# Performance work log

Hardware: AMD Instinct MI355X
Metric: run time of the kernel (lower is better)

The kernel has to match this reference:

```python
import jax, jax.numpy as jnp
import numpy as np

HIDDEN = 96
INF = 1e30


def setup_inputs() -> dict:
    key = jax.random.key(0)
    ks = jax.random.split(key, 9)
    B, JX, JM, D_IN, D_MEM = 8, 2048, 2048, 150, 150
    GATED = D_IN + D_MEM  # 300
    inputs = jax.random.normal(ks[0], (B, JX, D_IN), dtype=jnp.float32)
    memory = jax.random.normal(ks[1], (B, JM, D_MEM), dtype=jnp.float32)
    mask = jax.random.randint(ks[2], (B, JM), 0, 2, dtype=jnp.int32)
    s_in = 1.0 / np.sqrt(D_IN)
    s_g = 1.0 / np.sqrt(GATED)
    Wi = jax.random.uniform(ks[3], (D_IN, HIDDEN), jnp.float32, -s_in, s_in)
    bi = jax.random.uniform(ks[4], (HIDDEN,), jnp.float32, -s_in, s_in)
    Wm = jax.random.uniform(ks[5], (D_MEM, HIDDEN), jnp.float32, -s_in, s_in)
    bm = jax.random.uniform(ks[6], (HIDDEN,), jnp.float32, -s_in, s_in)
    Wg = jax.random.uniform(ks[7], (GATED, GATED), jnp.float32, -s_g, s_g)
    bg = jax.random.uniform(ks[8], (GATED,), jnp.float32, -s_g, s_g)
    return {"inputs": inputs, "memory": memory, "mask": mask,
            "Wi": Wi, "bi": bi, "Wm": Wm, "bm": bm, "Wg": Wg, "bg": bg}


def reference(inputs, memory, mask, Wi, bi, Wm, bm, Wg, bg):
    # ReLU projections (inference mode: dropout is identity)
    inputs_ = jax.nn.relu(jnp.einsum('bxd,dh->bxh', inputs, Wi) + bi)  # [B,JX,H]
    memory_ = jax.nn.relu(jnp.einsum('byd,dh->byh', memory, Wm) + bm)  # [B,JM,H]
    # Scaled dot-product scores [B,JX,JM]
    scores = jnp.einsum('bxh,byh->bxy', inputs_, memory_) / jnp.sqrt(
        jnp.asarray(HIDDEN, inputs.dtype))
    # Additive mask: -INF where mask==0 (broadcast over JX)
    maskf = mask.astype(inputs.dtype)[:, None, :]  # [B,1,JM]
    scores = scores - INF * (1.0 - maskf)
    logits = jax.nn.softmax(scores, axis=-1)
    outputs = jnp.einsum('bxy,byd->bxd', logits, memory)  # [B,JX,D_MEM]
    res = jnp.concatenate([inputs, outputs], axis=2)  # [B,JX,GATED]
    gate = jax.nn.sigmoid(jnp.einsum('bxg,gk->bxk', res, Wg) + bg)
    return gate * res
```

## Files before the change

### kernel.cpp

```cpp
#include <hip/hip_runtime.h>

#define BB 8
#define JX 2048
#define JMDIM 2048
#define DID 150
#define HID 96
#define GATED 300
#define NSPLIT 2
#define NROWS (BB * JX)

typedef unsigned short u16;
typedef __attribute__((ext_vector_type(8))) short bh8;
typedef __attribute__((ext_vector_type(4))) float f32x4;

#define SCALE2    (0.14724444f)

__device__ inline float b2f(u16 u) {
    union { unsigned int i; float f; } c; c.i = ((unsigned int)u) << 16; return c.f;
}
__device__ inline u16 f2b(float f) {
    unsigned int u = __float_as_uint(f);
    unsigned int r = (u + 0x7fffu + ((u >> 16) & 1u)) >> 16;
    return (u16)r;
}

__global__ __launch_bounds__(256) void proj2_kernel(
    const float* __restrict__ inputs, const float* __restrict__ memory,
    const int* __restrict__ mask,
    const float* __restrict__ Wi, const float* __restrict__ bi,
    const float* __restrict__ Wm, const float* __restrict__ bm,
    const float* __restrict__ Wg,
    u16* __restrict__ Qp, u16* __restrict__ Xi,
    u16* __restrict__ Kp, u16* __restrict__ Vt,
    u16* __restrict__ Wgt, int* __restrict__ mcount) {
    __shared__ __align__(16) u16 Xl[64 * 168];
    __shared__ __align__(16) u16 Wl[96 * 168];
    __shared__ int Il[64];
    __shared__ int wsum[4];
    const int tid = threadIdx.x;

    if (blockIdx.y == 2) {
        int t = blockIdx.x * 256 + tid;
        for (int e = t; e < 304 * 328; e += 256 * 256) {
            int k = e / 328, d = e - k * 328;
            Wgt[e] = (k < GATED && d < GATED) ? f2b(Wg[d * GATED + k]) : (u16)0;
        }
        return;
    }

    if (blockIdx.y == 0) {
        size_t row0 = (size_t)blockIdx.x * 64;
        const float4* Xv = (const float4*)(inputs + row0 * DID);
        for (int i = tid; i < 2400; i += 256) {
            float4 v = Xv[i];
            int base = i * 4;
#pragma unroll
            for (int k = 0; k < 4; ++k) {
                int id = base + k;
                int r = id / DID, d = id - r * DID;
                Xl[r * 168 + d] = f2b(((const float*)&v)[k]);
            }
        }
        for (int e = tid; e < 64 * 18; e += 256) {
            int r = e / 18, d = 150 + (e - r * 18);
            Xl[r * 168 + d] = 0;
        }
        for (int e = tid; e < 96 * 168; e += 256) {
            int h = e / 168, d = e - h * 168;
            Wl[e] = (d < DID) ? f2b(Wi[d * HID + h]) : (u16)0;
        }
        __syncthreads();

        for (int e = tid; e < 64 * 20; e += 256) {
            int r = e / 20, c = e - r * 20;
            *(bh8*)(Xi + (row0 + r) * 160 + c * 8) = *(const bh8*)(Xl + r * 168 + c * 8);
        }

        int wave = tid >> 6, lane = tid & 63, quad = lane >> 4, l15 = lane & 15;
        bh8 af[5];
#pragma unroll
        for (int kc = 0; kc < 5; ++kc)
            af[kc] = *(const bh8*)(Xl + (wave * 16 + l15) * 168 + kc * 32 + quad * 8);
#pragma unroll
        for (int nt = 0; nt < 6; ++nt) {
            f32x4 acc = {0.f, 0.f, 0.f, 0.f};
#pragma unroll
            for (int kc = 0; kc < 5; ++kc) {
                bh8 bf = *(const bh8*)(Wl + (nt * 16 + l15) * 168 + kc * 32 + quad * 8);
                acc = __builtin_amdgcn_mfma_f32_16x16x32_bf16(af[kc], bf, acc, 0, 0, 0);
            }
            int h = nt * 16 + l15;
            float bv = bi[h];
#pragma unroll
            for (int j = 0; j < 4; ++j) {
                float y = acc[j] + bv;
                y = y > 0.f ? y : 0.f;
                Qp[(row0 + wave * 16 + quad * 4 + j) * HID + h] = f2b(y);
            }
        }
        return;
    }

    const int b = blockIdx.x >> 5, s = blockIdx.x & 31;
    const int jc0 = s * 64;

    const int* m = mask + (size_t)b * JMDIM;
    int v[8], cnt = 0;
#pragma unroll
    for (int k = 0; k < 8; ++k) { v[k] = m[tid * 8 + k]; cnt += v[k]; }
    {
        int lane = tid & 63, wave = tid >> 6;
        int sc = cnt;
        for (int off = 1; off < 64; off <<= 1) {
            int t = __shfl_up(sc, off, 64);
            if (lane >= off) sc += t;
        }
        if (lane == 63) wsum[wave] = sc;
        if (tid < 64) Il[tid] = -1;
        __syncthreads();
        int wbase = 0;
        for (int w = 0; w < wave; ++w) wbase += wsum[w];
        int base = wbase + sc - cnt;
        int mc_ = wsum[0] + wsum[1] + wsum[2] + wsum[3];
        if (s == 0 && tid == 0) mcount[b] = mc_;
        int p = base;
#pragma unroll
        for (int k = 0; k < 8; ++k) {
            if (v[k]) {
                unsigned off = (unsigned)(p - jc0);
                if (off < 64u) Il[off] = tid * 8 + k;
                ++p;
            }
        }
        for (int e = tid; e < 96 * 168; e += 256) {
            int h = e / 168, d = e - h * 168;
            Wl[e] = (d < DID) ? f2b(Wm[d * HID + h]) : (u16)0;
        }
        __syncthreads();
        const int ntiles = (mc_ + 63) >> 6;
        if (s >= ntiles) return;
    }
    const int mc = wsum[0] + wsum[1] + wsum[2] + wsum[3];

    const float* Mb = memory + (size_t)b * JMDIM * DID;
    for (int e = tid; e < 64 * 75; e += 256) {
        int r = e / 75, c = e - r * 75;
        int row = Il[r];
        float2 val = make_float2(0.f, 0.f);
        if (row >= 0) val = *(const float2*)(Mb + (size_t)row * DID + c * 2);
        Xl[r * 168 + c * 2]     = f2b(val.x);
        Xl[r * 168 + c * 2 + 1] = f2b(val.y);
    }
    for (int e = tid; e < 64 * 18; e += 256) {
        int r = e / 18, d = 150 + (e - r * 18);
        Xl[r * 168 + d] = 0;
    }
    __syncthreads();

    for (int e = tid; e < 160 * 64; e += 256) {
        int d = e >> 6, c = e & 63;
        int jc = jc0 + c;
        u16 vv;
        if (d < DID)       vv = Xl[c * 168 + d];
        else if (d == DID) vv = (jc < mc) ? (u16)0x3F80 : (u16)0;
        else               vv = 0;
        Vt[((size_t)b * 160 + d) * JMDIM + jc] = vv;
    }

    int wave = tid >> 6, lane = tid & 63, quad = lane >> 4, l15 = lane & 15;
    bh8 af[5];
#pragma unroll
    for (int kc = 0; kc < 5; ++kc)
        af[kc] = *(const bh8*)(Xl + (wave * 16 + l15) * 168 + kc * 32 + quad * 8);
#pragma unroll
    for (int nt = 0; nt < 6; ++nt) {
        f32x4 acc = {0.f, 0.f, 0.f, 0.f};
#pragma unroll
        for (int kc = 0; kc < 5; ++kc) {
            bh8 bf = *(const bh8*)(Wl + (nt * 16 + l15) * 168 + kc * 32 + quad * 8);
            acc = __builtin_amdgcn_mfma_f32_16x16x32_bf16(af[kc], bf, acc, 0, 0, 0);
        }
        int h = nt * 16 + l15;
        float bv = bm[h];
#pragma unroll
        for (int j = 0; j < 4; ++j) {
            float y = acc[j] + bv;
            y = y > 0.f ? y : 0.f;
            Kp[((size_t)b * JMDIM + jc0 + wave * 16 + quad * 4 + j) * HID + h] = f2b(y);
        }
    }
}

template <int SPLIT>
__global__ __launch_bounds__(256, 2) void attn_kernel(
    const u16* __restrict__ Qp, const u16* __restrict__ Kp,
    const u16* __restrict__ Vt, const int* __restrict__ mcount,
    u16* __restrict__ Opart, float* __restrict__ lpart) {
    __shared__ __align__(16) u16 Kl[64 * 104];
    __shared__ __align__(16) u16 Vl[160 * 72];
    __shared__ __align__(16) u16 Pl[128 * 72];
    const int b = blockIdx.y;
    const int x0 = blockIdx.x * 128;
    const int tid = threadIdx.x;
    const int wave = tid >> 6, lane = tid & 63;
    const int quad = lane >> 4, l15 = lane & 15;

    const int mc = mcount[b];
    const int ntiles = (mc + 63) >> 6;
    const int zi = blockIdx.z;
    const int myT = (ntiles > zi) ? ((ntiles - 1 - zi) / SPLIT + 1) : 0;

    bh8 qf[2][3];
#pragma unroll
    for (int mt = 0; mt < 2; ++mt) {
        const u16* qb = Qp + ((size_t)b * JX + x0 + wave * 32 + mt * 16 + l15) * HID + quad * 8;
        qf[mt][0] = *(const bh8*)(qb);
        qf[mt][1] = *(const bh8*)(qb + 32);
        qf[mt][2] = *(const bh8*)(qb + 64);
    }

    f32x4 o[2][10];
    const f32x4 zero4 = {0.f, 0.f, 0.f, 0.f};
#pragma unroll
    for (int mt = 0; mt < 2; ++mt)
#pragma unroll
        for (int i = 0; i < 10; ++i) o[mt][i] = zero4;

    const int jm0_0 = zi * 64;

    const u16* kptr[3]; u16* kdst[3];
#pragma unroll
    for (int t = 0; t < 3; ++t) {
        int i = tid + t * 256, r = i / 12, c = i - r * 12;
        kptr[t] = Kp + ((size_t)b * JMDIM + jm0_0 + r) * HID + c * 8;
        kdst[t] = Kl + r * 104 + c * 8;
    }
    const u16* vptr[5]; u16* vdst[5];
#pragma unroll
    for (int t = 0; t < 5; ++t) {
        int i = tid + t * 256, d = i >> 3, c = i & 7;
        vptr[t] = Vt + ((size_t)b * 160 + d) * JMDIM + jm0_0 + c * 8;
        vdst[t] = Vl + d * 72 + c * 8;
    }

    bh8 kreg[3], vreg[5];
    if (myT > 0) {
#pragma unroll
        for (int t = 0; t < 3; ++t) { kreg[t] = *(const bh8*)kptr[t]; kptr[t] += SPLIT * 64 * HID; }
#pragma unroll
        for (int t = 0; t < 5; ++t) { vreg[t] = *(const bh8*)vptr[t]; vptr[t] += SPLIT * 64; }
    }

    for (int it = 0; it < myT; ++it) {
        __syncthreads();
#pragma unroll
        for (int t = 0; t < 3; ++t) *(bh8*)kdst[t] = kreg[t];
#pragma unroll
        for (int t = 0; t < 5; ++t) *(bh8*)vdst[t] = vreg[t];
        if (it + 1 < myT) {
#pragma unroll
            for (int t = 0; t < 3; ++t) { kreg[t] = *(const bh8*)kptr[t]; kptr[t] += SPLIT * 64 * HID; }
#pragma unroll
            for (int t = 0; t < 5; ++t) { vreg[t] = *(const bh8*)vptr[t]; vptr[t] += SPLIT * 64; }
        }
        __syncthreads();

        f32x4 s[2][4];
#pragma unroll
        for (int mt = 0; mt < 2; ++mt)
#pragma unroll
            for (int nt = 0; nt < 4; ++nt) s[mt][nt] = zero4;
#pragma unroll
        for (int nt = 0; nt < 4; ++nt) {
#pragma unroll
            for (int kc = 0; kc < 3; ++kc) {
                bh8 bf = *(const bh8*)(Kl + (nt * 16 + l15) * 104 + kc * 32 + quad * 8);
                s[0][nt] = __builtin_amdgcn_mfma_f32_16x16x32_bf16(qf[0][kc], bf, s[0][nt], 0, 0, 0);
                s[1][nt] = __builtin_amdgcn_mfma_f32_16x16x32_bf16(qf[1][kc], bf, s[1][nt], 0, 0, 0);
            }
        }
#pragma unroll
        for (int nt = 0; nt < 4; ++nt) {
#pragma unroll
            for (int mt = 0; mt < 2; ++mt)
#pragma unroll
                for (int j = 0; j < 4; ++j) {
                    float p = __builtin_amdgcn_exp2f(s[mt][nt][j] * SCALE2);
                    Pl[(wave * 32 + mt * 16 + quad * 4 + j) * 72 + nt * 16 + l15] = f2b(p);
                }
        }
        __threadfence_block();

        bh8 pf[2][2];
#pragma unroll
        for (int mt = 0; mt < 2; ++mt) {
            pf[mt][0] = *(const bh8*)(Pl + (wave * 32 + mt * 16 + l15) * 72 + quad * 8);
            pf[mt][1] = *(const bh8*)(Pl + (wave * 32 + mt * 16 + l15) * 72 + 32 + quad * 8);
        }
#pragma unroll
        for (int nt = 0; nt < 10; ++nt) {
#pragma unroll
            for (int kc = 0; kc < 2; ++kc) {
                bh8 bf = *(const bh8*)(Vl + (nt * 16 + l15) * 72 + kc * 32 + quad * 8);
                o[0][nt] = __builtin_amdgcn_mfma_f32_16x16x32_bf16(pf[0][kc], bf, o[0][nt], 0, 0, 0);
                o[1][nt] = __builtin_amdgcn_mfma_f32_16x16x32_bf16(pf[1][kc], bf, o[1][nt], 0, 0, 0);
            }
        }
    }

    const size_t z = blockIdx.z;
    const int srcLane = (lane & 48) | 6;
#pragma unroll
    for (int mt = 0; mt < 2; ++mt) {
        float lv[4], inv[4];
#pragma unroll
        for (int j = 0; j < 4; ++j) {
            lv[j] = __shfl(o[mt][9][j], srcLane, 64);
            inv[j] = (lv[j] > 0.f) ? 1.f / lv[j] : 0.f;
        }
        size_t grow = (size_t)b * JX + x0 + wave * 32 + mt * 16;
#pragma unroll
        for (int nt = 0; nt < 10; ++nt) {
            int d = nt * 16 + l15;
            if (d < 152) {
#pragma unroll
                for (int j = 0; j < 4; ++j)
                    Opart[(z * NROWS + grow + quad * 4 + j) * 152 + d] = f2b(o[mt][nt][j] * inv[j]);
            }
        }
        if (l15 == 0) {
#pragma unroll
            for (int j = 0; j < 4; ++j)
                lpart[z * NROWS + grow + quad * 4 + j] = lv[j];
        }
    }
}

template <int SPLIT>
__global__ __launch_bounds__(256) void gate_kernel(
    const u16* __restrict__ Xi, const u16* __restrict__ Opart,
    const float* __restrict__ lpart,
    const u16* __restrict__ Wgt, const float* __restrict__ bg,
    float* __restrict__ out) {
    __shared__ __align__(16) u16 Rl[32 * 328];
    __shared__ float Cw[SPLIT * 32];
    int tid = threadIdx.x;
    size_t row0 = (size_t)blockIdx.x * 32;

    if (tid < 32) {
        float l[SPLIT], L = 0.f;
#pragma unroll
        for (int s = 0; s < SPLIT; ++s) {
            l[s] = lpart[(size_t)s * NROWS + row0 + tid];
            L += l[s];
        }
        float invL = (L > 0.f) ? 1.f / L : 0.f;
#pragma unroll
        for (int s = 0; s < SPLIT; ++s) Cw[s * 32 + tid] = l[s] * invL;
    }
    for (int e = tid; e < 32 * 20; e += 256) {
        int r = e / 20, c = e - r * 20;
        *(bh8*)(Rl + r * 328 + c * 8) = *(const bh8*)(Xi + (row0 + r) * 160 + c * 8);
    }
    __syncthreads();
    for (int e = tid; e < 32 * 19; e += 256) {
        int r = e / 19, q = e - r * 19;
        float acc[8];
#pragma unroll
        for (int k = 0; k < 8; ++k) acc[k] = 0.f;
#pragma unroll
        for (int s = 0; s < SPLIT; ++s) {
            bh8 v = *(const bh8*)(Opart + ((size_t)s * NROWS + row0 + r) * 152 + q * 8);
            float w = Cw[s * 32 + r];
#pragma unroll
            for (int k = 0; k < 8; ++k) acc[k] += b2f(((const u16*)&v)[k]) * w;
        }
        u16* dst = Rl + r * 328 + 150 + q * 8;
#pragma unroll
        for (int k = 0; k < 8; ++k) dst[k] = f2b(acc[k]);
    }
    for (int e = tid; e < 32 * 26; e += 256) {
        int r = e / 26, c = 302 + (e - r * 26);
        Rl[r * 328 + c] = 0;
    }
    __syncthreads();

    int wave = tid >> 6, lane = tid & 63, quad = lane >> 4, l15 = lane & 15;
    bh8 af[2][10];
#pragma unroll
    for (int mt = 0; mt < 2; ++mt)
#pragma unroll
        for (int kc = 0; kc < 10; ++kc)
            af[mt][kc] = *(const bh8*)(Rl + (mt * 16 + l15) * 328 + kc * 32 + quad * 8);
    for (int nt = wave; nt < 19; nt += 4) {
        int h = nt * 16 + l15;
        f32x4 acc0 = {0.f, 0.f, 0.f, 0.f};
        f32x4 acc1 = {0.f, 0.f, 0.f, 0.f};
#pragma unroll
        for (int kc = 0; kc < 10; ++kc) {
            bh8 bf = *(const bh8*)(Wgt + (size_t)h * 328 + kc * 32 + quad * 8);
            acc0 = __builtin_amdgcn_mfma_f32_16x16x32_bf16(af[0][kc], bf, acc0, 0, 0, 0);
            acc1 = __builtin_amdgcn_mfma_f32_16x16x32_bf16(af[1][kc], bf, acc1, 0, 0, 0);
        }
        if (h < GATED) {
            float bv = bg[h];
#pragma unroll
            for (int j = 0; j < 4; ++j) {
                int r0 = quad * 4 + j;
                float x0 = acc0[j] + bv;
                float g0 = 1.f / (1.f + __expf(-x0));
                out[(row0 + r0) * GATED + h] = g0 * b2f(Rl[r0 * 328 + h]);
                int r1 = r0 + 16;
                float x1 = acc1[j] + bv;
                float g1 = 1.f / (1.f + __expf(-x1));
                out[(row0 + r1) * GATED + h] = g1 * b2f(Rl[r1 * 328 + h]);
            }
        }
    }
}

extern "C" void kernel_launch(void* const* d_in, const int* in_sizes, int n_in,
                              void* d_out, int out_size, void* d_ws, size_t ws_size,
                              hipStream_t stream) {
    const float* inputs = (const float*)d_in[0];
    const float* memory = (const float*)d_in[1];
    const int*   mask   = (const int*)d_in[2];
    const float* Wi = (const float*)d_in[3];
    const float* bi = (const float*)d_in[4];
    const float* Wm = (const float*)d_in[5];
    const float* bm = (const float*)d_in[6];
    const float* Wg = (const float*)d_in[7];
    const float* bg = (const float*)d_in[8];
    float* out = (float*)d_out;

    u16* Qp  = (u16*)d_ws;
    u16* Kp  = Qp + (size_t)NROWS * HID;
    u16* Vt  = Kp + (size_t)NROWS * HID;
    u16* Xi  = Vt + (size_t)BB * 160 * JMDIM;
    u16* Wgt = Xi + (size_t)NROWS * 160;
    u16* Opart = Wgt + 304 * 328;
    size_t u16_elems = (size_t)(Opart - Qp) + (size_t)NSPLIT * NROWS * 152;
    size_t base_bytes = ((u16_elems * sizeof(u16)) + 15) & ~(size_t)15;
    float* lpart = (float*)((char*)d_ws + base_bytes);
    int* mcountp = (int*)(lpart + (size_t)NSPLIT * NROWS);
    size_t needed = base_bytes + (size_t)NSPLIT * NROWS * sizeof(float)
                  + BB * sizeof(int);
    if (ws_size < needed) return;

    proj2_kernel<<<dim3(256, 3), 256, 0, stream>>>(
        inputs, memory, mask, Wi, bi, Wm, bm, Wg,
        Qp, Xi, Kp, Vt, Wgt, mcountp);
    attn_kernel<NSPLIT><<<dim3(JX / 128, BB, NSPLIT), 256, 0, stream>>>(
        Qp, Kp, Vt, mcountp, Opart, lpart);
    gate_kernel<NSPLIT><<<dim3(NROWS / 32), 256, 0, stream>>>(
        Xi, Opart, lpart, Wgt, bg, out);
}
```

Before: 150.9 us.

## Halve attention query tile to 64 rows and coalesce weight loads in projection

The attention kernel now processes 64 query rows per block (one 16-row MFMA tile per wave) instead of 128, doubling the grid and halving per-wave registers and P shared memory. This aims to raise occupancy and spread work over more CUs, at the cost of loading each K/V tile twice as often per query row. The projection kernel now reads Wi/Wm row-major (coalesced) and scatters the transpose into LDS with a separate padding loop. exp2 also switches from the builtin to exp2f.

```diff
diff --git a/kernel.cpp b/kernel.cpp
--- a/kernel.cpp
+++ b/kernel.cpp
@@ -65,9 +65,13 @@
             int r = e / 18, d = 150 + (e - r * 18);
             Xl[r * 168 + d] = 0;
         }
-        for (int e = tid; e < 96 * 168; e += 256) {
-            int h = e / 168, d = e - h * 168;
-            Wl[e] = (d < DID) ? f2b(Wi[d * HID + h]) : (u16)0;
+        for (int e = tid; e < DID * HID; e += 256) {
+            int d = e / HID, h = e - d * HID;
+            Wl[h * 168 + d] = f2b(Wi[e]);
+        }
+        for (int e = tid; e < HID * 18; e += 256) {
+            int h = e / 18, d = 150 + (e - h * 18);
+            Wl[h * 168 + d] = 0;
         }
         __syncthreads();
 
@@ -108,6 +112,7 @@
     int v[8], cnt = 0;
 #pragma unroll
     for (int k = 0; k < 8; ++k) { v[k] = m[tid * 8 + k]; cnt += v[k]; }
+    int mc;
     {
         int lane = tid & 63, wave = tid >> 6;
         int sc = cnt;
@@ -121,8 +126,8 @@
         int wbase = 0;
         for (int w = 0; w < wave; ++w) wbase += wsum[w];
         int base = wbase + sc - cnt;
-        int mc_ = wsum[0] + wsum[1] + wsum[2] + wsum[3];
-        if (s == 0 && tid == 0) mcount[b] = mc_;
+        mc = wsum[0] + wsum[1] + wsum[2] + wsum[3];
+        if (s == 0 && tid == 0) mcount[b] = mc;
         int p = base;
 #pragma unroll
         for (int k = 0; k < 8; ++k) {
@@ -132,15 +137,18 @@
                 ++p;
             }
         }
-        for (int e = tid; e < 96 * 168; e += 256) {
-            int h = e / 168, d = e - h * 168;
-            Wl[e] = (d < DID) ? f2b(Wm[d * HID + h]) : (u16)0;
+        for (int e = tid; e < DID * HID; e += 256) {
+            int d = e / HID, h = e - d * HID;
+            Wl[h * 168 + d] = f2b(Wm[e]);
+        }
+        for (int e = tid; e < HID * 18; e += 256) {
+            int h = e / 18, d = 150 + (e - h * 18);
+            Wl[h * 168 + d] = 0;
         }
         __syncthreads();
-        const int ntiles = (mc_ + 63) >> 6;
+        const int ntiles = (mc + 63) >> 6;
         if (s >= ntiles) return;
     }
-    const int mc = wsum[0] + wsum[1] + wsum[2] + wsum[3];
 
     const float* Mb = memory + (size_t)b * JMDIM * DID;
     for (int e = tid; e < 64 * 75; e += 256) {
@@ -198,9 +206,9 @@
     u16* __restrict__ Opart, float* __restrict__ lpart) {
     __shared__ __align__(16) u16 Kl[64 * 104];
     __shared__ __align__(16) u16 Vl[160 * 72];
-    __shared__ __align__(16) u16 Pl[128 * 72];
+    __shared__ __align__(16) u16 Pl[64 * 72];
     const int b = blockIdx.y;
-    const int x0 = blockIdx.x * 128;
+    const int x0 = blockIdx.x * 64;
     const int tid = threadIdx.x;
     const int wave = tid >> 6, lane = tid & 63;
     const int quad = lane >> 4, l15 = lane & 15;
@@ -210,21 +218,18 @@
     const int zi = blockIdx.z;
     const int myT = (ntiles > zi) ? ((ntiles - 1 - zi) / SPLIT + 1) : 0;
 
-    bh8 qf[2][3];
-#pragma unroll
-    for (int mt = 0; mt < 2; ++mt) {
-        const u16* qb = Qp + ((size_t)b * JX + x0 + wave * 32 + mt * 16 + l15) * HID + quad * 8;
-        qf[mt][0] = *(const bh8*)(qb);
-        qf[mt][1] = *(const bh8*)(qb + 32);
-        qf[mt][2] = *(const bh8*)(qb + 64);
-    }
-
-    f32x4 o[2][10];
+    bh8 qf[3];
+    {
+        const u16* qb = Qp + ((size_t)b * JX + x0 + wave * 16 + l15) * HID + quad * 8;
+        qf[0] = *(const bh8*)(qb);
+        qf[1] = *(const bh8*)(qb + 32);
+        qf[2] = *(const bh8*)(qb + 64);
+    }
+
+    f32x4 o[10];
     const f32x4 zero4 = {0.f, 0.f, 0.f, 0.f};
 #pragma unroll
-    for (int mt = 0; mt < 2; ++mt)
-#pragma unroll
-        for (int i = 0; i < 10; ++i) o[mt][i] = zero4;
+    for (int i = 0; i < 10; ++i) o[i] = zero4;
 
     const int jm0_0 = zi * 64;
 
@@ -265,74 +270,62 @@
         }
         __syncthreads();
 
-        f32x4 s[2][4];
-#pragma unroll
-        for (int mt = 0; mt < 2; ++mt)
-#pragma unroll
-            for (int nt = 0; nt < 4; ++nt) s[mt][nt] = zero4;
+        f32x4 s[4];
+#pragma unroll
+        for (int nt = 0; nt < 4; ++nt) s[nt] = zero4;
 #pragma unroll
         for (int nt = 0; nt < 4; ++nt) {
 #pragma unroll
             for (int kc = 0; kc < 3; ++kc) {
                 bh8 bf = *(const bh8*)(Kl + (nt * 16 + l15) * 104 + kc * 32 + quad * 8);
-                s[0][nt] = __builtin_amdgcn_mfma_f32_16x16x32_bf16(qf[0][kc], bf, s[0][nt], 0, 0, 0);
-                s[1][nt] = __builtin_amdgcn_mfma_f32_16x16x32_bf16(qf[1][kc], bf, s[1][nt], 0, 0, 0);
+                s[nt] = __builtin_amdgcn_mfma_f32_16x16x32_bf16(qf[kc], bf, s[nt], 0, 0, 0);
             }
         }
 #pragma unroll
         for (int nt = 0; nt < 4; ++nt) {
 #pragma unroll
-            for (int mt = 0; mt < 2; ++mt)
-#pragma unroll
-                for (int j = 0; j < 4; ++j) {
-                    float p = __builtin_amdgcn_exp2f(s[mt][nt][j] * SCALE2);
-                    Pl[(wave * 32 + mt * 16 + quad * 4 + j) * 72 + nt * 16 + l15] = f2b(p);
-                }
+            for (int j = 0; j < 4; ++j) {
+                float p = exp2f(s[nt][j] * SCALE2);
+                Pl[(wave * 16 + quad * 4 + j) * 72 + nt * 16 + l15] = f2b(p);
+            }
         }
         __threadfence_block();
 
-        bh8 pf[2][2];
-#pragma unroll
-        for (int mt = 0; mt < 2; ++mt) {
-            pf[mt][0] = *(const bh8*)(Pl + (wave * 32 + mt * 16 + l15) * 72 + quad * 8);
-            pf[mt][1] = *(const bh8*)(Pl + (wave * 32 + mt * 16 + l15) * 72 + 32 + quad * 8);
-        }
+        bh8 pf[2];
+        pf[0] = *(const bh8*)(Pl + (wave * 16 + l15) * 72 + quad * 8);
+        pf[1] = *(const bh8*)(Pl + (wave * 16 + l15) * 72 + 32 + quad * 8);
 #pragma unroll
         for (int nt = 0; nt < 10; ++nt) {
 #pragma unroll
             for (int kc = 0; kc < 2; ++kc) {
                 bh8 bf = *(const bh8*)(Vl + (nt * 16 + l15) * 72 + kc * 32 + quad * 8);
-                o[0][nt] = __builtin_amdgcn_mfma_f32_16x16x32_bf16(pf[0][kc], bf, o[0][nt], 0, 0, 0);
-                o[1][nt] = __builtin_amdgcn_mfma_f32_16x16x32_bf16(pf[1][kc], bf, o[1][nt], 0, 0, 0);
+                o[nt] = __builtin_amdgcn_mfma_f32_16x16x32_bf16(pf[kc], bf, o[nt], 0, 0, 0);
             }
         }
     }
 
     const size_t z = blockIdx.z;
     const int srcLane = (lane & 48) | 6;
-#pragma unroll
-    for (int mt = 0; mt < 2; ++mt) {
-        float lv[4], inv[4];
-#pragma unroll
-        for (int j = 0; j < 4; ++j) {
-            lv[j] = __shfl(o[mt][9][j], srcLane, 64);
-            inv[j] = (lv[j] > 0.f) ? 1.f / lv[j] : 0.f;
-        }
-        size_t grow = (size_t)b * JX + x0 + wave * 32 + mt * 16;
-#pragma unroll
-        for (int nt = 0; nt < 10; ++nt) {
-            int d = nt * 16 + l15;
-            if (d < 152) {
-#pragma unroll
-                for (int j = 0; j < 4; ++j)
-                    Opart[(z * NROWS + grow + quad * 4 + j) * 152 + d] = f2b(o[mt][nt][j] * inv[j]);
-            }
-        }
-        if (l15 == 0) {
+    float lv[4], inv[4];
+#pragma unroll
+    for (int j = 0; j < 4; ++j) {
+        lv[j] = __shfl(o[9][j], srcLane, 64);
+        inv[j] = (lv[j] > 0.f) ? 1.f / lv[j] : 0.f;
+    }
+    size_t grow = (size_t)b * JX + x0 + wave * 16;
+#pragma unroll
+    for (int nt = 0; nt < 10; ++nt) {
+        int d = nt * 16 + l15;
+        if (d < 152) {
 #pragma unroll
             for (int j = 0; j < 4; ++j)
-                lpart[z * NROWS + grow + quad * 4 + j] = lv[j];
-        }
+                Opart[(z * NROWS + grow + quad * 4 + j) * 152 + d] = f2b(o[nt][j] * inv[j]);
+        }
+    }
+    if (l15 == 0) {
+#pragma unroll
+        for (int j = 0; j < 4; ++j)
+            lpart[z * NROWS + grow + quad * 4 + j] = lv[j];
     }
 }
 
@@ -450,7 +443,7 @@
     proj2_kernel<<<dim3(256, 3), 256, 0, stream>>>(
         inputs, memory, mask, Wi, bi, Wm, bm, Wg,
         Qp, Xi, Kp, Vt, Wgt, mcountp);
-    attn_kernel<NSPLIT><<<dim3(JX / 128, BB, NSPLIT), 256, 0, stream>>>(
+    attn_kernel<NSPLIT><<<dim3(JX / 64, BB, NSPLIT), 256, 0, stream>>>(
         Qp, Kp, Vt, mcountp, Opart, lpart);
     gate_kernel<NSPLIT><<<dim3(NROWS / 32), 256, 0, stream>>>(
         Xi, Opart, lpart, Wgt, bg, out);
```

New measurement: 140.7 us. 1.07x faster.
